# Kernel tuning notes

Measured on AMD Instinct MI355X. Metric: run time of the kernel, lower is better.

The kernel has to match this reference:

```python
import jax, jax.numpy as jnp
import numpy as np

EMBED = 1024
HEADS = 16
HEAD_DIM = EMBED // HEADS
B, N = 2, 2048


def setup_inputs() -> dict:
    key = jax.random.key(0)
    ks = jax.random.split(key, 7)
    s = 1.0 / np.sqrt(EMBED)
    x = jax.random.normal(ks[0], (B, N, EMBED), dtype=jnp.float32)
    # causal mask: 1 where attention allowed, 0 elsewhere (masked_fill on mask==0)
    mask = jnp.tril(jnp.ones((N, N), dtype=jnp.int32))[None, None, :, :]
    Wq = jax.random.uniform(ks[1], (EMBED, EMBED), jnp.float32, -s, s)
    Wk = jax.random.uniform(ks[2], (EMBED, EMBED), jnp.float32, -s, s)
    Wv = jax.random.uniform(ks[3], (EMBED, EMBED), jnp.float32, -s, s)
    Wo = jax.random.uniform(ks[4], (EMBED, EMBED), jnp.float32, -s, s)
    bo = jax.random.uniform(ks[5], (EMBED,), jnp.float32, -s, s)
    return {"x": x, "mask": mask, "Wq": Wq, "Wk": Wk, "Wv": Wv, "Wo": Wo, "bo": bo}


def reference(x, mask, Wq, Wk, Wv, Wo, bo):
    Bx, Nx, D = x.shape
    # torch nn.Linear: y = x @ W.T
    q = (x @ Wq.T).reshape(Bx, Nx, HEADS, HEAD_DIM).transpose(0, 2, 1, 3)
    k = (x @ Wk.T).reshape(Bx, Nx, HEADS, HEAD_DIM).transpose(0, 2, 1, 3)
    v = (x @ Wv.T).reshape(Bx, Nx, HEADS, HEAD_DIM).transpose(0, 2, 1, 3)
    score = jnp.einsum('bhqd,bhkd->bhqk', q, k) / np.sqrt(HEAD_DIM).astype(np.float32)
    score = jnp.where(mask == 0, -jnp.inf, score)
    probs = jax.nn.softmax(score, axis=-1)
    out = jnp.einsum('bhqk,bhkd->bhqd', probs, v)  # [B,H,N,hd]
    out = out.transpose(0, 2, 1, 3).reshape(Bx, Nx, D)
    return out @ Wo.T + bo
```

## Files before the change

kernel.cpp:

```cpp
#include <hip/hip_runtime.h>
#include <hip/hip_bf16.h>

#define B_  2
#define N_  2048
#define E_  1024
#define H_  16
#define HD_ 64
#define M_  (B_*N_)
#define RSZ ((size_t)M_ * E_)

typedef short bf16x8 __attribute__((ext_vector_type(8)));
typedef float f32x4 __attribute__((ext_vector_type(4)));
typedef unsigned short u16x8 __attribute__((ext_vector_type(8)));

#define AS1 __attribute__((address_space(1)))
#define AS3 __attribute__((address_space(3)))

__device__ __forceinline__ unsigned short f2bfu(float f) {
    __hip_bfloat16 h = __float2bfloat16(f);
    return *reinterpret_cast<unsigned short*>(&h);
}
__device__ __forceinline__ unsigned int cvtpk(float lo, float hi) {
    unsigned int r;
    asm("v_cvt_pk_bf16_f32 %0, %1, %2" : "=v"(r) : "v"(lo), "v"(hi));
    return r;
}
#define MFMA16(a,b,c) __builtin_amdgcn_mfma_f32_16x16x32_bf16((a),(b),(c),0,0,0)

__device__ __forceinline__ void gl_lds16(const void* g, void* l) {
    __builtin_amdgcn_global_load_lds((const AS1 void*)g, (AS3 void*)l, 16, 0, 0);
}

__global__ __launch_bounds__(256) void fconv_all_kernel(
    const float* __restrict__ x,
    const float* __restrict__ Wq, const float* __restrict__ Wk,
    const float* __restrict__ Wv, const float* __restrict__ Wo,
    unsigned short* __restrict__ xbf, unsigned short* __restrict__ wbf)
{
    const int bid = blockIdx.x;
    const float* src;
    unsigned short* dst;
    int off;
    if (bid < 2048) {
        src = x; dst = xbf; off = bid * 2048 + threadIdx.x * 8;
    } else {
        const int z = (bid - 2048) >> 9;
        src = (z == 0) ? Wq : (z == 1 ? Wk : (z == 2 ? Wv : Wo));
        dst = wbf + (size_t)z * E_ * E_;
        off = ((bid - 2048) & 511) * 2048 + threadIdx.x * 8;
    }
    const float4 a = *reinterpret_cast<const float4*>(src + off);
    const float4 b = *reinterpret_cast<const float4*>(src + off + 4);
    u16x8 v;
    v[0]=f2bfu(a.x); v[1]=f2bfu(a.y); v[2]=f2bfu(a.z); v[3]=f2bfu(a.w);
    v[4]=f2bfu(b.x); v[5]=f2bfu(b.y); v[6]=f2bfu(b.z); v[7]=f2bfu(b.w);
    *reinterpret_cast<u16x8*>(dst + off) = v;
}

__global__ __launch_bounds__(256) void fconv_kernel(
    const float* __restrict__ src, unsigned short* __restrict__ dst)
{
    const int i0 = (blockIdx.x * 256 + threadIdx.x) * 8;
    const float4 a = *reinterpret_cast<const float4*>(src + i0);
    const float4 b = *reinterpret_cast<const float4*>(src + i0 + 4);
    u16x8 v;
    v[0]=f2bfu(a.x); v[1]=f2bfu(a.y); v[2]=f2bfu(a.z); v[3]=f2bfu(a.w);
    v[4]=f2bfu(b.x); v[5]=f2bfu(b.y); v[6]=f2bfu(b.z); v[7]=f2bfu(b.w);
    *reinterpret_cast<u16x8*>(dst + i0) = v;
}

__global__ __launch_bounds__(256) void qkv_fused_kernel(
    const unsigned short* __restrict__ xbf, const unsigned short* __restrict__ wbf,
    unsigned short* __restrict__ qkv)
{
    const int m0 = blockIdx.x * 64;
    const int n0 = blockIdx.y * 128;
    __shared__ unsigned short ldsA[64*64];
    __shared__ unsigned short ldsB[3][128*64];
    const int t = threadIdx.x;
    const int lane = t & 63;
    const int w = t >> 6, wr = w >> 1, wc = w & 1;
    const int fr = lane & 15, fq = lane >> 4;
    const int subrow = lane >> 3;
    const int csw = ((lane & 7) ^ subrow) * 8;
    const int rcol = ((fq * 8) ^ ((fr & 7) * 8));
    f32x4 acc[3][2][4] = {};

    for (int kt = 0; kt < 16; ++kt) {
        const int k0 = kt * 64;
        __syncthreads();
        #pragma unroll
        for (int i = 0; i < 14; ++i) {
            const int c = w * 14 + i;
            if (c < 8) {
                const int row = c * 8 + subrow;
                gl_lds16(xbf + (size_t)(m0 + row) * E_ + k0 + csw, &ldsA[c * 512]);
            } else {
                const int cc = c - 8;
                const int zb = cc >> 4, bc = cc & 15;
                const int row = bc * 8 + subrow;
                gl_lds16(wbf + (size_t)zb * E_ * E_ + (size_t)(n0 + row) * E_ + k0 + csw,
                         &ldsB[zb][bc * 512]);
            }
        }
        __syncthreads();
        #pragma unroll
        for (int ks = 0; ks < 2; ++ks) {
            bf16x8 af[2];
            #pragma unroll
            for (int mf = 0; mf < 2; ++mf)
                af[mf] = *(const bf16x8*)&ldsA[(wr*32 + mf*16 + fr)*64 + (rcol ^ (ks*32))];
            #pragma unroll
            for (int zb = 0; zb < 3; ++zb) {
                bf16x8 bfv[4];
                #pragma unroll
                for (int nf = 0; nf < 4; ++nf)
                    bfv[nf] = *(const bf16x8*)&ldsB[zb][(wc*64 + nf*16 + fr)*64 + (rcol ^ (ks*32))];
                #pragma unroll
                for (int mf = 0; mf < 2; ++mf)
                    #pragma unroll
                    for (int nf = 0; nf < 4; ++nf)
                        acc[zb][mf][nf] = MFMA16(af[mf], bfv[nf], acc[zb][mf][nf]);
            }
        }
    }

    #pragma unroll
    for (int zb = 0; zb < 3; ++zb) {
        unsigned short* __restrict__ out = qkv + (size_t)zb * RSZ;
        const float scale = (zb == 0) ? 0.125f : 1.0f;
        #pragma unroll
        for (int mf = 0; mf < 2; ++mf) {
            #pragma unroll
            for (int r = 0; r < 4; ++r) {
                const int m = m0 + wr*32 + mf*16 + fq*4 + r;
                const int b = m >> 11, npos = m & (N_ - 1);
                #pragma unroll
                for (int nf = 0; nf < 4; ++nf) {
                    const int n = n0 + wc*64 + nf*16 + fr;
                    const int h = n >> 6, d = n & 63;
                    const unsigned short val = f2bfu(acc[zb][mf][nf][r] * scale);
                    if (zb == 2)
                        out[(((size_t)(b*H_ + h))*HD_ + d)*N_ + npos] = val;
                    else
                        out[(((size_t)(b*H_ + h))*N_ + npos)*HD_ + d] = val;
                }
            }
        }
    }
}

__global__ __launch_bounds__(256) void qkv_f32_kernel(
    const float* __restrict__ x, const unsigned short* __restrict__ wbf,
    unsigned short* __restrict__ qkv)
{
    const int z = blockIdx.z;
    const unsigned short* __restrict__ W = wbf + (size_t)z * E_ * E_;
    unsigned short* __restrict__ out = qkv + (size_t)z * RSZ;
    const int m0 = blockIdx.x * 128;
    const int n0 = blockIdx.y * 128;
    __shared__ unsigned short As[128][72];
    __shared__ unsigned short Bs[128][72];
    const int t = threadIdx.x;
    const int lane = t & 63;
    const int w = t >> 6, wr = w >> 1, wc = w & 1;
    const int fr = lane & 15, fq = lane >> 4;
    const int srow = t >> 1, scol = (t & 1) * 32;
    f32x4 acc[4][4] = {};

    const float* arow = x + (size_t)(m0 + srow) * E_ + scol;
    const unsigned short* brow = W + (size_t)(n0 + srow) * E_ + scol;

    float4 a4[8];
    u16x8 b8[4];
    #pragma unroll
    for (int i = 0; i < 8; ++i) a4[i] = reinterpret_cast<const float4*>(arow)[i];
    #pragma unroll
    for (int i = 0; i < 4; ++i) b8[i] = reinterpret_cast<const u16x8*>(brow)[i];

    for (int k0 = 0; k0 < E_; k0 += 64) {
        __syncthreads();
        #pragma unroll
        for (int j = 0; j < 4; ++j) {
            u16x8 va;
            va[0]=f2bfu(a4[2*j].x); va[1]=f2bfu(a4[2*j].y); va[2]=f2bfu(a4[2*j].z); va[3]=f2bfu(a4[2*j].w);
            va[4]=f2bfu(a4[2*j+1].x); va[5]=f2bfu(a4[2*j+1].y); va[6]=f2bfu(a4[2*j+1].z); va[7]=f2bfu(a4[2*j+1].w);
            *reinterpret_cast<u16x8*>(&As[srow][scol + 8*j]) = va;
            *reinterpret_cast<u16x8*>(&Bs[srow][scol + 8*j]) = b8[j];
        }
        __syncthreads();
        if (k0 + 64 < E_) {
            #pragma unroll
            for (int i = 0; i < 8; ++i)
                a4[i] = reinterpret_cast<const float4*>(arow + k0 + 64)[i];
            #pragma unroll
            for (int i = 0; i < 4; ++i)
                b8[i] = reinterpret_cast<const u16x8*>(brow + k0 + 64)[i];
        }
        #pragma unroll
        for (int ks = 0; ks < 2; ++ks) {
            bf16x8 af[4], bfv[4];
            #pragma unroll
            for (int mf = 0; mf < 4; ++mf)
                af[mf] = *reinterpret_cast<const bf16x8*>(&As[wr*64 + mf*16 + fr][ks*32 + fq*8]);
            #pragma unroll
            for (int nf = 0; nf < 4; ++nf)
                bfv[nf] = *reinterpret_cast<const bf16x8*>(&Bs[wc*64 + nf*16 + fr][ks*32 + fq*8]);
            #pragma unroll
            for (int mf = 0; mf < 4; ++mf)
                #pragma unroll
                for (int nf = 0; nf < 4; ++nf)
                    acc[mf][nf] = MFMA16(af[mf], bfv[nf], acc[mf][nf]);
        }
    }

    const float scale = (z == 0) ? 0.125f : 1.0f;
    #pragma unroll
    for (int mf = 0; mf < 4; ++mf) {
        #pragma unroll
        for (int r = 0; r < 4; ++r) {
            const int m = m0 + wr*64 + mf*16 + fq*4 + r;
            const int b = m >> 11, npos = m & (N_ - 1);
            #pragma unroll
            for (int nf = 0; nf < 4; ++nf) {
                const int n = n0 + wc*64 + nf*16 + fr;
                const int h = n >> 6, d = n & 63;
                const unsigned short val = f2bfu(acc[mf][nf][r] * scale);
                if (z == 2)
                    out[(((size_t)(b*H_ + h))*HD_ + d)*N_ + npos] = val;
                else
                    out[(((size_t)(b*H_ + h))*N_ + npos)*HD_ + d] = val;
            }
        }
    }
}

__global__ __launch_bounds__(256) void attn_mfma_kernel(
    const unsigned short* __restrict__ qkv, unsigned short* __restrict__ attn_out)
{
    const int bh = blockIdx.x;
    const int qt = (int)(gridDim.y - 1) - (int)blockIdx.y;
    const unsigned short* Qp  = qkv + (size_t)bh * N_ * HD_;
    const unsigned short* Kp  = qkv + RSZ + (size_t)bh * N_ * HD_;
    const unsigned short* Vtp = qkv + 2*RSZ + (size_t)bh * N_ * HD_;
    __shared__ unsigned short Ks[128][72], Vt[64][136];
    const int t = threadIdx.x;
    const int lane = t & 63, w = t >> 6;
    const int fr = lane & 15, fq = lane >> 4;
    const int srK = t >> 1, scK = (t & 1) * 32;
    const int srV = t >> 2, scV = (t & 3) * 32;
    const int qbase = qt * 64 + w * 16;
    const int KT = (qt * 64 + 63) / 128 + 1;
    const int ql = qbase + fr;
    const int lane_b0 = (2 * (fq & 1)) * 16 + fr;
    const int lane_b1 = lane_b0 + 16;
    const bool hi_sel = (fq >> 1) != 0;

    bf16x8 qfr[2];
    #pragma unroll
    for (int ks = 0; ks < 2; ++ks)
        qfr[ks] = *reinterpret_cast<const bf16x8*>(
            Qp + (size_t)ql * HD_ + ks*32 + fq*8);

    float m_run = -1e30f, l_run = 0.f;
    f32x4 o[4] = {};

    u16x8 kr[4], vr[4];
    #pragma unroll
    for (int j = 0; j < 4; ++j) {
        kr[j] = *reinterpret_cast<const u16x8*>(Kp + (size_t)srK * HD_ + scK + 8*j);
        vr[j] = *reinterpret_cast<const u16x8*>(Vtp + (size_t)srV * N_ + scV + 8*j);
    }

    for (int kt = 0; kt < KT; ++kt) {
        const int k0 = kt * 128;
        __syncthreads();
        #pragma unroll
        for (int j = 0; j < 4; ++j) {
            *reinterpret_cast<u16x8*>(&Ks[srK][scK + 8*j]) = kr[j];
            *reinterpret_cast<u16x8*>(&Vt[srV][scV + 8*j]) = vr[j];
        }
        __syncthreads();
        if (kt + 1 < KT) {
            const int kn = k0 + 128;
            #pragma unroll
            for (int j = 0; j < 4; ++j) {
                kr[j] = *reinterpret_cast<const u16x8*>(Kp + (size_t)(kn + srK) * HD_ + scK + 8*j);
                vr[j] = *reinterpret_cast<const u16x8*>(Vtp + (size_t)srV * N_ + kn + scV + 8*j);
            }
        }
        if (k0 > qbase + 15) continue;

        f32x4 s[8] = {};
        __builtin_amdgcn_s_setprio(1);
        #pragma unroll
        for (int ks = 0; ks < 2; ++ks) {
            #pragma unroll
            for (int nf = 0; nf < 8; ++nf) {
                bf16x8 bk = *reinterpret_cast<const bf16x8*>(&Ks[nf*16 + fr][ks*32 + fq*8]);
                s[nf] = MFMA16(bk, qfr[ks], s[nf]);
            }
        }
        __builtin_amdgcn_s_setprio(0);

        if (k0 + 127 > qbase) {
            #pragma unroll
            for (int nf = 0; nf < 8; ++nf)
                #pragma unroll
                for (int r = 0; r < 4; ++r)
                    if (k0 + nf*16 + fq*4 + r > ql) s[nf][r] = -1e30f;
        }

        float pm = -1e30f;
        #pragma unroll
        for (int nf = 0; nf < 8; ++nf)
            pm = fmaxf(pm, fmaxf(fmaxf(s[nf][0], s[nf][1]),
                                 fmaxf(s[nf][2], s[nf][3])));
        pm = fmaxf(pm, __shfl_xor(pm, 16));
        pm = fmaxf(pm, __shfl_xor(pm, 32));

        const bool need = __any(pm > m_run + 8.f);
        float scl = 1.f;
        if (need) {
            const float mnew = fmaxf(m_run, pm);
            scl = __expf(m_run - mnew);
            m_run = mnew;
        }

        float rs = 0.f;
        unsigned int u[8][2];
        #pragma unroll
        for (int nf = 0; nf < 8; ++nf) {
            const float p0 = __expf(s[nf][0] - m_run);
            const float p1 = __expf(s[nf][1] - m_run);
            const float p2 = __expf(s[nf][2] - m_run);
            const float p3 = __expf(s[nf][3] - m_run);
            rs += (p0 + p1) + (p2 + p3);
            u[nf][0] = cvtpk(p0, p1);
            u[nf][1] = cvtpk(p2, p3);
        }
        {
            float v = rs;
            v += __shfl_xor(v, 16);
            v += __shfl_xor(v, 32);
            l_run = l_run * scl + v;
        }
        if (need) {
            #pragma unroll
            for (int df = 0; df < 4; ++df)
                #pragma unroll
                for (int r = 0; r < 4; ++r)
                    o[df][r] *= scl;
        }

        bf16x8 pb[4];
        #pragma unroll
        for (int kk = 0; kk < 4; ++kk) {
            const unsigned int t00 = __shfl(u[2*kk+0][0], lane_b0);
            const unsigned int t01 = __shfl(u[2*kk+0][1], lane_b0);
            const unsigned int t02 = __shfl(u[2*kk+0][0], lane_b1);
            const unsigned int t03 = __shfl(u[2*kk+0][1], lane_b1);
            const unsigned int t10 = __shfl(u[2*kk+1][0], lane_b0);
            const unsigned int t11 = __shfl(u[2*kk+1][1], lane_b0);
            const unsigned int t12 = __shfl(u[2*kk+1][0], lane_b1);
            const unsigned int t13 = __shfl(u[2*kk+1][1], lane_b1);
            union { unsigned int wd[4]; bf16x8 v; } pu;
            pu.wd[0] = hi_sel ? t10 : t00;
            pu.wd[1] = hi_sel ? t11 : t01;
            pu.wd[2] = hi_sel ? t12 : t02;
            pu.wd[3] = hi_sel ? t13 : t03;
            pb[kk] = pu.v;
        }

        __builtin_amdgcn_s_setprio(1);
        #pragma unroll
        for (int kk = 0; kk < 4; ++kk) {
            bf16x8 bv[4];
            #pragma unroll
            for (int df = 0; df < 4; ++df)
                bv[df] = *reinterpret_cast<const bf16x8*>(&Vt[df*16 + fr][kk*32 + fq*8]);
            #pragma unroll
            for (int df = 0; df < 4; ++df)
                o[df] = MFMA16(bv[df], pb[kk], o[df]);
        }
        __builtin_amdgcn_s_setprio(0);
    }

    const int b = bh >> 4, h = bh & 15;
    const float inv = 1.0f / l_run;
    #pragma unroll
    for (int df = 0; df < 4; ++df)
        #pragma unroll
        for (int r = 0; r < 4; ++r) {
            const int d = df*16 + fq*4 + r;
            attn_out[((size_t)(b*N_ + ql))*E_ + h*64 + d] = f2bfu(o[df][r] * inv);
        }
}

__global__ __launch_bounds__(256) void out_glds_kernel(
    const unsigned short* __restrict__ A, const unsigned short* __restrict__ Wobf,
    const float* __restrict__ bo, float* __restrict__ out)
{
    const int m0 = blockIdx.x * 64;
    const int n0 = blockIdx.y * 128;
    __shared__ unsigned short ldsA[64*64];
    __shared__ unsigned short ldsB[128*64];
    const int t = threadIdx.x;
    const int lane = t & 63;
    const int w = t >> 6, wr = w >> 1, wc = w & 1;
    const int fr = lane & 15, fq = lane >> 4;
    const int subrow = lane >> 3;
    const int csw = ((lane & 7) ^ subrow) * 8;
    const int rcol = ((fq * 8) ^ ((fr & 7) * 8));
    f32x4 acc[2][4] = {};

    for (int kt = 0; kt < 16; ++kt) {
        const int k0 = kt * 64;
        __syncthreads();
        #pragma unroll
        for (int i = 0; i < 6; ++i) {
            const int c = w * 6 + i;
            if (c < 8) {
                const int row = c * 8 + subrow;
                gl_lds16(A + (size_t)(m0 + row) * E_ + k0 + csw, &ldsA[c * 512]);
            } else {
                const int row = (c - 8) * 8 + subrow;
                gl_lds16(Wobf + (size_t)(n0 + row) * E_ + k0 + csw, &ldsB[(c - 8) * 512]);
            }
        }
        __syncthreads();
        #pragma unroll
        for (int ks = 0; ks < 2; ++ks) {
            bf16x8 af[2], bfv[4];
            #pragma unroll
            for (int mf = 0; mf < 2; ++mf)
                af[mf] = *(const bf16x8*)&ldsA[(wr*32 + mf*16 + fr)*64 + (rcol ^ (ks*32))];
            #pragma unroll
            for (int nf = 0; nf < 4; ++nf)
                bfv[nf] = *(const bf16x8*)&ldsB[(wc*64 + nf*16 + fr)*64 + (rcol ^ (ks*32))];
            #pragma unroll
            for (int mf = 0; mf < 2; ++mf)
                #pragma unroll
                for (int nf = 0; nf < 4; ++nf)
                    acc[mf][nf] = MFMA16(af[mf], bfv[nf], acc[mf][nf]);
        }
    }

    #pragma unroll
    for (int mf = 0; mf < 2; ++mf) {
        #pragma unroll
        for (int r = 0; r < 4; ++r) {
            const int m = m0 + wr*32 + mf*16 + fq*4 + r;
            #pragma unroll
            for (int nf = 0; nf < 4; ++nf) {
                const int n = n0 + wc*64 + nf*16 + fr;
                out[(size_t)m * E_ + n] = acc[mf][nf][r] + bo[n];
            }
        }
    }
}

extern "C" void kernel_launch(void* const* d_in, const int* in_sizes, int n_in,
                              void* d_out, int out_size, void* d_ws, size_t ws_size,
                              hipStream_t stream) {
    const float* x  = (const float*)d_in[0];
    const float* Wq = (const float*)d_in[2];
    const float* Wk = (const float*)d_in[3];
    const float* Wv = (const float*)d_in[4];
    const float* Wo = (const float*)d_in[5];
    const float* bo = (const float*)d_in[6];
    float* out = (float*)d_out;

    unsigned short* ws = (unsigned short*)d_ws;
    const size_t need_main = 5 * RSZ * sizeof(unsigned short);

    if (ws_size >= need_main) {
        unsigned short* xbf  = ws;
        unsigned short* wbf  = ws + RSZ;
        unsigned short* qkvq = ws + 2 * RSZ;
        unsigned short* attn_ws = ws;
        unsigned short* wobf = wbf + 3 * (size_t)E_ * E_;

        fconv_all_kernel<<<4096, 256, 0, stream>>>(x, Wq, Wk, Wv, Wo, xbf, wbf);

        dim3 g1(M_ / 64, E_ / 128);
        qkv_fused_kernel<<<g1, 256, 0, stream>>>(xbf, wbf, qkvq);

        dim3 g2(B_ * H_, N_ / 64);
        attn_mfma_kernel<<<g2, 256, 0, stream>>>(qkvq, attn_ws);

        dim3 g3(M_ / 64, E_ / 128);
        out_glds_kernel<<<g3, 256, 0, stream>>>(attn_ws, wobf, bo, out);
    } else {
        unsigned short* wbf = ws;
        unsigned short* qkvq = ws + RSZ;
        unsigned short* attn_ws = ws;
        unsigned short* wobf = ws + RSZ;

        const int cgrid = E_ * E_ / (256 * 8);
        fconv_kernel<<<cgrid, 256, 0, stream>>>(Wq, wbf);
        fconv_kernel<<<cgrid, 256, 0, stream>>>(Wk, wbf + (size_t)E_ * E_);
        fconv_kernel<<<cgrid, 256, 0, stream>>>(Wv, wbf + 2 * (size_t)E_ * E_);

        dim3 g1(M_ / 128, E_ / 128, 3);
        qkv_f32_kernel<<<g1, 256, 0, stream>>>(x, wbf, qkvq);

        dim3 g2(B_ * H_, N_ / 64);
        attn_mfma_kernel<<<g2, 256, 0, stream>>>(qkvq, attn_ws);

        fconv_kernel<<<cgrid, 256, 0, stream>>>(Wo, wobf);

        dim3 g3(M_ / 64, E_ / 128);
        out_glds_kernel<<<g3, 256, 0, stream>>>(attn_ws, wobf, bo, out);
    }
}
```

Before: 109.9 us.

## Read K and V fragments directly from global memory in attention kernel

Removes the shared-memory staging of K and V tiles, along with the register prefetch and both block barriers per tile. Each wave now loads its MFMA operands straight from global memory, relying on L2/L1 caching for the reuse across the four waves. The key-tile count becomes per-wave, so each wave runs only as many tiles as its own causal extent, and launch bounds now request four blocks per CU. The cost is more global and cache traffic and exposed load latency, since there is no explicit prefetch.

```diff
diff --git a/kernel.cpp b/kernel.cpp
--- a/kernel.cpp
+++ b/kernel.cpp
@@ -235,22 +235,19 @@
     }
 }
 
-__global__ __launch_bounds__(256) void attn_mfma_kernel(
+__global__ __launch_bounds__(256, 4) void attn_mfma_kernel(
     const unsigned short* __restrict__ qkv, unsigned short* __restrict__ attn_out)
 {
     const int bh = blockIdx.x;
-    const int qt = (int)(gridDim.y - 1) - (int)blockIdx.y;
+    const int qt = 31 - (int)blockIdx.y;
     const unsigned short* Qp  = qkv + (size_t)bh * N_ * HD_;
     const unsigned short* Kp  = qkv + RSZ + (size_t)bh * N_ * HD_;
     const unsigned short* Vtp = qkv + 2*RSZ + (size_t)bh * N_ * HD_;
-    __shared__ unsigned short Ks[128][72], Vt[64][136];
     const int t = threadIdx.x;
     const int lane = t & 63, w = t >> 6;
     const int fr = lane & 15, fq = lane >> 4;
-    const int srK = t >> 1, scK = (t & 1) * 32;
-    const int srV = t >> 2, scV = (t & 3) * 32;
     const int qbase = qt * 64 + w * 16;
-    const int KT = (qt * 64 + 63) / 128 + 1;
+    const int KT = (qbase + 15) / 128 + 1;
     const int ql = qbase + fr;
     const int lane_b0 = (2 * (fq & 1)) * 16 + fr;
     const int lane_b1 = lane_b0 + 16;
@@ -265,41 +262,21 @@
     float m_run = -1e30f, l_run = 0.f;
     f32x4 o[4] = {};
 
-    u16x8 kr[4], vr[4];
-    #pragma unroll
-    for (int j = 0; j < 4; ++j) {
-        kr[j] = *reinterpret_cast<const u16x8*>(Kp + (size_t)srK * HD_ + scK + 8*j);
-        vr[j] = *reinterpret_cast<const u16x8*>(Vtp + (size_t)srV * N_ + scV + 8*j);
-    }
-
     for (int kt = 0; kt < KT; ++kt) {
         const int k0 = kt * 128;
-        __syncthreads();
-        #pragma unroll
-        for (int j = 0; j < 4; ++j) {
-            *reinterpret_cast<u16x8*>(&Ks[srK][scK + 8*j]) = kr[j];
-            *reinterpret_cast<u16x8*>(&Vt[srV][scV + 8*j]) = vr[j];
-        }
-        __syncthreads();
-        if (kt + 1 < KT) {
-            const int kn = k0 + 128;
-            #pragma unroll
-            for (int j = 0; j < 4; ++j) {
-                kr[j] = *reinterpret_cast<const u16x8*>(Kp + (size_t)(kn + srK) * HD_ + scK + 8*j);
-                vr[j] = *reinterpret_cast<const u16x8*>(Vtp + (size_t)srV * N_ + kn + scV + 8*j);
-            }
-        }
-        if (k0 > qbase + 15) continue;
 
         f32x4 s[8] = {};
         __builtin_amdgcn_s_setprio(1);
         #pragma unroll
         for (int ks = 0; ks < 2; ++ks) {
-            #pragma unroll
-            for (int nf = 0; nf < 8; ++nf) {
-                bf16x8 bk = *reinterpret_cast<const bf16x8*>(&Ks[nf*16 + fr][ks*32 + fq*8]);
-                s[nf] = MFMA16(bk, qfr[ks], s[nf]);
-            }
+            bf16x8 bk[8];
+            #pragma unroll
+            for (int nf = 0; nf < 8; ++nf)
+                bk[nf] = *reinterpret_cast<const bf16x8*>(
+                    Kp + (size_t)(k0 + nf*16 + fr) * HD_ + ks*32 + fq*8);
+            #pragma unroll
+            for (int nf = 0; nf < 8; ++nf)
+                s[nf] = MFMA16(bk[nf], qfr[ks], s[nf]);
         }
         __builtin_amdgcn_s_setprio(0);
 
@@ -378,7 +355,8 @@
             bf16x8 bv[4];
             #pragma unroll
             for (int df = 0; df < 4; ++df)
-                bv[df] = *reinterpret_cast<const bf16x8*>(&Vt[df*16 + fr][kk*32 + fq*8]);
+                bv[df] = *reinterpret_cast<const bf16x8*>(
+                    Vtp + (size_t)(df*16 + fr) * N_ + k0 + kk*32 + fq*8);
             #pragma unroll
             for (int df = 0; df < 4; ++df)
                 o[df] = MFMA16(bv[df], pb[kk], o[df]);
@@ -486,7 +464,7 @@
         dim3 g1(M_ / 64, E_ / 128);
         qkv_fused_kernel<<<g1, 256, 0, stream>>>(xbf, wbf, qkvq);
 
-        dim3 g2(B_ * H_, N_ / 64);
+        dim3 g2(B_ * H_, 32);
         attn_mfma_kernel<<<g2, 256, 0, stream>>>(qkvq, attn_ws);
 
         dim3 g3(M_ / 64, E_ / 128);
@@ -505,7 +483,7 @@
         dim3 g1(M_ / 128, E_ / 128, 3);
         qkv_f32_kernel<<<g1, 256, 0, stream>>>(x, wbf, qkvq);
 
-        dim3 g2(B_ * H_, N_ / 64);
+        dim3 g2(B_ * H_, 32);
         attn_mfma_kernel<<<g2, 256, 0, stream>>>(qkvq, attn_ws);
 
         fconv_kernel<<<cgrid, 256, 0, stream>>>(Wo, wobf);
```

New measurement: 205.8 us. 87.2% more time.
